# Performance work log

Hardware: AMD Instinct MI355X
Metric: run time of the kernel (lower is better)

The kernel has to match this reference:

```python
import jax, jax.numpy as jnp
import numpy as np

N_NODES = 100000
N_EDGES = 1600000
D_IN = 128
D_OUT = 128


def setup_inputs() -> dict:
    key = jax.random.key(0)
    k1, k2, k3 = jax.random.split(key, 3)
    x = jax.random.normal(k1, (N_NODES, D_IN), dtype=jnp.float32)
    edge_index = jax.random.randint(k2, (2, N_EDGES), 0, N_NODES, dtype=jnp.int64)
    # Xavier-uniform-like init for weight (matches nn.init.xavier_uniform_ scale)
    limit = float(np.sqrt(6.0 / (D_IN + D_OUT)))
    weight = jax.random.uniform(k3, (D_IN, D_OUT), dtype=jnp.float32,
                                minval=-limit, maxval=limit)
    bias = jnp.zeros((D_OUT,), dtype=jnp.float32)
    return {"x": x, "edge_index": edge_index, "weight": weight, "bias": bias}


def reference(x, edge_index, weight, bias):
    num_nodes = x.shape[0]
    src = edge_index[0]  # edge_index_i: gather side
    dst = edge_index[1]  # edge_index_j: scatter side

    # Degree of each node counted over src endpoints.
    deg = jax.ops.segment_sum(jnp.ones_like(src, dtype=x.dtype), src,
                              num_segments=num_nodes)
    # deg^{-1/2} with inf -> 0 for isolated nodes.
    deg_safe = jnp.where(deg > 0, deg, jnp.ones_like(deg))
    deg_inv_sqrt = jnp.where(deg > 0, jax.lax.rsqrt(deg_safe), jnp.zeros_like(deg))

    norm = deg_inv_sqrt[src] * deg_inv_sqrt[dst]  # [E]

    h = x @ weight  # [N, D_OUT]
    # Edge-parallel gather, scale, scatter-add.
    msgs = norm[:, None] * h[src]  # [E, D_OUT]
    out = jax.ops.segment_sum(msgs, dst, num_segments=num_nodes)  # [N, D_OUT]
    return out + bias
```

## Files before the change

kernel.cpp:

```cpp
#include <hip/hip_runtime.h>

#define D 128
#define CAP 64
#define STRIP_LOG 13
#define STRIP (1 << STRIP_LOG)
#define NCHUNK 32
#define LDK 132

typedef __attribute__((ext_vector_type(8))) short bf16x8;
typedef __attribute__((ext_vector_type(4))) float f32x4;

__device__ __forceinline__ unsigned f2bf(float f) {
    unsigned u = __float_as_uint(f);
    return (u + 0x7fffu + ((u >> 16) & 1u)) >> 16;
}

__device__ __forceinline__ int chunk_size(int n_edges) {
    return (((n_edges + NCHUNK - 1) / NCHUNK) + 3) & ~3;
}

__global__ __launch_bounds__(256) void k_histA(const int* __restrict__ src,
                                               const int* __restrict__ dst,
                                               int* __restrict__ pb_s,
                                               int* __restrict__ pb_d, int n_edges) {
    int strip = blockIdx.x / NCHUNK, chunk = blockIdx.x % NCHUNK;
    int lo = strip << STRIP_LOG;
    __shared__ int hs[STRIP];
    __shared__ int hd[STRIP];
    for (int i = threadIdx.x; i < STRIP; i += 256) { hs[i] = 0; hd[i] = 0; }
    __syncthreads();

    int csz = chunk_size(n_edges);
    int beg = chunk * csz;
    int end = min(beg + csz, n_edges);
    if (beg < end) {
        int aend = beg + ((end - beg) & ~3);
        for (int i = beg + threadIdx.x * 4; i + 3 < aend; i += 1024) {
            int4 s = *(const int4*)(src + i);
            int4 d = *(const int4*)(dst + i);
            unsigned b;
            b = (unsigned)(s.x - lo); if (b < STRIP) atomicAdd(&hs[b], 1);
            b = (unsigned)(s.y - lo); if (b < STRIP) atomicAdd(&hs[b], 1);
            b = (unsigned)(s.z - lo); if (b < STRIP) atomicAdd(&hs[b], 1);
            b = (unsigned)(s.w - lo); if (b < STRIP) atomicAdd(&hs[b], 1);
            b = (unsigned)(d.x - lo); if (b < STRIP) atomicAdd(&hd[b], 1);
            b = (unsigned)(d.y - lo); if (b < STRIP) atomicAdd(&hd[b], 1);
            b = (unsigned)(d.z - lo); if (b < STRIP) atomicAdd(&hd[b], 1);
            b = (unsigned)(d.w - lo); if (b < STRIP) atomicAdd(&hd[b], 1);
        }
        for (int e = aend + threadIdx.x; e < end; e += 256) {
            unsigned bs = (unsigned)(src[e] - lo); if (bs < STRIP) atomicAdd(&hs[bs], 1);
            unsigned bd = (unsigned)(dst[e] - lo); if (bd < STRIP) atomicAdd(&hd[bd], 1);
        }
    }
    __syncthreads();
    int* ps = pb_s + (size_t)blockIdx.x * STRIP;
    int* pd = pb_d + (size_t)blockIdx.x * STRIP;
    for (int i = threadIdx.x; i < STRIP; i += 256) { ps[i] = hs[i]; pd[i] = hd[i]; }
}

__global__ __launch_bounds__(256) void k_base_dis(int* __restrict__ pb_d,
                                                  const int* __restrict__ pb_s,
                                                  int* __restrict__ deg_dst,
                                                  float* __restrict__ dis,
                                                  int n, int nbins) {
    int g = blockIdx.x * 256 + threadIdx.x;
    if (g >= nbins) return;
    int strip = g >> STRIP_LOG, bin = g & (STRIP - 1);
    size_t base = (size_t)strip * NCHUNK * STRIP + bin;
    int run = 0;
    #pragma unroll
    for (int c = 0; c < NCHUNK; ++c) {
        size_t idx = base + (size_t)c * STRIP;
        int v = pb_d[idx];
        pb_d[idx] = run;
        run += v;
    }
    if (g < n) {
        deg_dst[g] = run;
        int ssum = 0;
        #pragma unroll
        for (int c = 0; c < NCHUNK; ++c) ssum += pb_s[base + (size_t)c * STRIP];
        dis[g] = (ssum > 0) ? rsqrtf((float)ssum) : 0.0f;
    }
}

__global__ __launch_bounds__(256) void k_placeB(const int* __restrict__ src,
                                                const int* __restrict__ dst,
                                                const int* __restrict__ pb_d,
                                                int* __restrict__ epad, int n_edges) {
    int strip = blockIdx.x / NCHUNK, chunk = blockIdx.x % NCHUNK;
    int lo = strip << STRIP_LOG;
    __shared__ int cur[STRIP];
    const int* cb = pb_d + (size_t)blockIdx.x * STRIP;
    for (int i = threadIdx.x; i < STRIP; i += 256) cur[i] = cb[i];
    __syncthreads();

    int csz = chunk_size(n_edges);
    int beg = chunk * csz;
    int end = min(beg + csz, n_edges);
    if (beg < end) {
        int aend = beg + ((end - beg) & ~3);
        for (int i = beg + threadIdx.x * 4; i + 3 < aend; i += 1024) {
            int4 s = *(const int4*)(src + i);
            int4 d = *(const int4*)(dst + i);
            unsigned b;
            b = (unsigned)(d.x - lo);
            if (b < STRIP) { int r = atomicAdd(&cur[b], 1); if (r < CAP) epad[(((unsigned)lo + b) << 6) + r] = s.x; }
            b = (unsigned)(d.y - lo);
            if (b < STRIP) { int r = atomicAdd(&cur[b], 1); if (r < CAP) epad[(((unsigned)lo + b) << 6) + r] = s.y; }
            b = (unsigned)(d.z - lo);
            if (b < STRIP) { int r = atomicAdd(&cur[b], 1); if (r < CAP) epad[(((unsigned)lo + b) << 6) + r] = s.z; }
            b = (unsigned)(d.w - lo);
            if (b < STRIP) { int r = atomicAdd(&cur[b], 1); if (r < CAP) epad[(((unsigned)lo + b) << 6) + r] = s.w; }
        }
        for (int e = aend + threadIdx.x; e < end; e += 256) {
            unsigned b = (unsigned)(dst[e] - lo);
            if (b < STRIP) { int r = atomicAdd(&cur[b], 1); if (r < CAP) epad[(((unsigned)lo + b) << 6) + r] = src[e]; }
        }
    }
}

__global__ __launch_bounds__(256) void k_gemm(const float* __restrict__ x,
                                              const float* __restrict__ w,
                                              const float* __restrict__ dis,
                                              unsigned* __restrict__ hb, int nrows) {
    __shared__ __align__(16) unsigned short smem[2][128][LDK];
    int tid = threadIdx.x;
    int row0 = blockIdx.x * 128;
    int nr = min(128, nrows - row0);

    {
        const float4* w4 = (const float4*)w;
        for (int i = tid; i < 128 * 32; i += 256) {
            int k = i >> 5, n0 = (i & 31) * 4;
            float4 v = w4[i];
            smem[1][n0 + 0][k] = (unsigned short)f2bf(v.x);
            smem[1][n0 + 1][k] = (unsigned short)f2bf(v.y);
            smem[1][n0 + 2][k] = (unsigned short)f2bf(v.z);
            smem[1][n0 + 3][k] = (unsigned short)f2bf(v.w);
        }
    }
    {
        const float4* x4 = (const float4*)(x + (size_t)row0 * D);
        for (int i = tid; i < 128 * 32; i += 256) {
            int r = i >> 5, c4 = (i & 31) * 4;
            float4 v = (r < nr) ? x4[i] : make_float4(0.f, 0.f, 0.f, 0.f);
            unsigned lo = f2bf(v.x) | (f2bf(v.y) << 16);
            unsigned hi = f2bf(v.z) | (f2bf(v.w) << 16);
            *(uint2*)&smem[0][r][c4] = make_uint2(lo, hi);
        }
    }
    __syncthreads();

    int lane = tid & 63, wv = tid >> 6;
    int m = lane & 15, quad = lane >> 4;
    int rbase = wv * 32;

    f32x4 acc[2][8] = {};
    #pragma unroll
    for (int kt = 0; kt < 4; ++kt) {
        int k0 = kt * 32 + quad * 8;
        bf16x8 a0 = *(const bf16x8*)&smem[0][rbase + m][k0];
        bf16x8 a1 = *(const bf16x8*)&smem[0][rbase + 16 + m][k0];
        bf16x8 b[8];
        #pragma unroll
        for (int ct = 0; ct < 8; ++ct)
            b[ct] = *(const bf16x8*)&smem[1][ct * 16 + m][k0];
        #pragma unroll
        for (int ct = 0; ct < 8; ++ct) {
            acc[0][ct] = __builtin_amdgcn_mfma_f32_16x16x32_bf16(a0, b[ct], acc[0][ct], 0, 0, 0);
            acc[1][ct] = __builtin_amdgcn_mfma_f32_16x16x32_bf16(a1, b[ct], acc[1][ct], 0, 0, 0);
        }
    }

    __syncthreads();
    float* sO = (float*)smem;
    #pragma unroll
    for (int rt = 0; rt < 2; ++rt)
        #pragma unroll
        for (int ct = 0; ct < 8; ++ct)
            #pragma unroll
            for (int reg = 0; reg < 4; ++reg)
                sO[(rbase + rt * 16 + quad * 4 + reg) * LDK + ct * 16 + m] = acc[rt][ct][reg];
    __syncthreads();

    int r = tid >> 1, hf = tid & 1;
    if (r < nr) {
        float dn = dis[row0 + r];
        const float* so = sO + r * LDK + hf * 64;
        unsigned* hrow = hb + (size_t)(row0 + r) * 64 + hf * 32;
        #pragma unroll
        for (int j = 0; j < 8; ++j) {
            float2 p0 = *(const float2*)(so + j * 8 + 0);
            float2 p1 = *(const float2*)(so + j * 8 + 2);
            float2 p2 = *(const float2*)(so + j * 8 + 4);
            float2 p3 = *(const float2*)(so + j * 8 + 6);
            uint4 o;
            o.x = f2bf(dn * p0.x) | (f2bf(dn * p0.y) << 16);
            o.y = f2bf(dn * p1.x) | (f2bf(dn * p1.y) << 16);
            o.z = f2bf(dn * p2.x) | (f2bf(dn * p2.y) << 16);
            o.w = f2bf(dn * p3.x) | (f2bf(dn * p3.y) << 16);
            *(uint4*)(hrow + j * 4) = o;
        }
    }
}

#define ACC8(u) do { \
    ax[0] += __uint_as_float((u).x << 16); ax[1] += __uint_as_float((u).x & 0xffff0000u); \
    ax[2] += __uint_as_float((u).y << 16); ax[3] += __uint_as_float((u).y & 0xffff0000u); \
    ax[4] += __uint_as_float((u).z << 16); ax[5] += __uint_as_float((u).z & 0xffff0000u); \
    ax[6] += __uint_as_float((u).w << 16); ax[7] += __uint_as_float((u).w & 0xffff0000u); } while (0)

__global__ __launch_bounds__(256) void k_accum(const int* __restrict__ epad,
                                               const int* __restrict__ degd,
                                               const uint4* __restrict__ hb4,
                                               const float* __restrict__ dis,
                                               const float* __restrict__ bias,
                                               float* __restrict__ out, int n) {
    int wid = threadIdx.x >> 6, lane = threadIdx.x & 63;
    int node = blockIdx.x * 4 + wid;
    if (node >= n) return;
    int deg = min(degd[node], CAP);
    int g = lane >> 4, c = lane & 15;
    const int* ep = epad + (size_t)node * CAP;

    float ax[8] = {0.f, 0.f, 0.f, 0.f, 0.f, 0.f, 0.f, 0.f};
    int e = g;
    for (; e + 12 < deg; e += 16) {
        int s0 = ep[e];
        int s1 = ep[e + 4];
        int s2 = ep[e + 8];
        int s3 = ep[e + 12];
        uint4 u0 = hb4[(size_t)s0 * 16 + c];
        uint4 u1 = hb4[(size_t)s1 * 16 + c];
        uint4 u2 = hb4[(size_t)s2 * 16 + c];
        uint4 u3 = hb4[(size_t)s3 * 16 + c];
        ACC8(u0); ACC8(u1); ACC8(u2); ACC8(u3);
    }
    for (; e < deg; e += 4) {
        int s0 = ep[e];
        uint4 u0 = hb4[(size_t)s0 * 16 + c];
        ACC8(u0);
    }

    #pragma unroll
    for (int k = 0; k < 8; ++k) {
        ax[k] += __shfl_xor(ax[k], 16, 64);
        ax[k] += __shfl_xor(ax[k], 32, 64);
    }

    if (g == 0) {
        float dn = dis[node];
        float4 b0 = ((const float4*)bias)[c * 2];
        float4 b1 = ((const float4*)bias)[c * 2 + 1];
        float4 o0 = make_float4(fmaf(dn, ax[0], b0.x), fmaf(dn, ax[1], b0.y),
                                fmaf(dn, ax[2], b0.z), fmaf(dn, ax[3], b0.w));
        float4 o1 = make_float4(fmaf(dn, ax[4], b1.x), fmaf(dn, ax[5], b1.y),
                                fmaf(dn, ax[6], b1.z), fmaf(dn, ax[7], b1.w));
        float4* op = (float4*)(out + (size_t)node * D) + c * 2;
        op[0] = o0;
        op[1] = o1;
    }
}

extern "C" void kernel_launch(void* const* d_in, const int* in_sizes, int n_in,
                              void* d_out, int out_size, void* d_ws, size_t ws_size,
                              hipStream_t stream) {
    const float* x    = (const float*)d_in[0];
    const int*   ei   = (const int*)d_in[1];
    const float* w    = (const float*)d_in[2];
    const float* bias = (const float*)d_in[3];
    float* out = (float*)d_out;

    int n_edges = in_sizes[1] / 2;
    int n_nodes = in_sizes[0] / D;
    const int* src = ei;
    const int* dst = ei + n_edges;

    int nstrips = (n_nodes + STRIP - 1) >> STRIP_LOG;
    int nbins = nstrips * STRIP;

    char* ws = (char*)d_ws;
    unsigned* hb = (unsigned*)ws;      ws += (size_t)n_nodes * 64 * sizeof(unsigned);
    int* epad    = (int*)ws;           ws += (size_t)n_nodes * CAP * sizeof(int);
    int* deg_dst = (int*)ws;           ws += (size_t)n_nodes * sizeof(int);
    float* dis   = (float*)ws;         ws += (size_t)n_nodes * sizeof(float);
    int* pb_s    = (int*)ws;           ws += (size_t)nstrips * NCHUNK * STRIP * sizeof(int);
    int* pb_d    = (int*)ws;

    k_histA<<<nstrips * NCHUNK, 256, 0, stream>>>(src, dst, pb_s, pb_d, n_edges);
    k_base_dis<<<(nbins + 255) / 256, 256, 0, stream>>>(pb_d, pb_s, deg_dst, dis,
                                                        n_nodes, nbins);
    k_gemm<<<(n_nodes + 127) / 128, 256, 0, stream>>>(x, w, dis, hb, n_nodes);
    k_placeB<<<nstrips * NCHUNK, 256, 0, stream>>>(src, dst, pb_d, epad, n_edges);
    k_accum<<<(n_nodes + 3) / 4, 256, 0, stream>>>(epad, deg_dst, (const uint4*)hb,
                                                   dis, bias, out, n_nodes);
}
```

Measured before the change: 283.0 us.

## Replace strip histogram and placement passes with single global-atomic placement kernel

Drops the strip-partitioned shared-memory histogram, prefix-base and placement kernels and replaces them with one edge-parallel kernel. It uses global atomics on per-node degree counters both to count source degrees and to assign slots in the padded destination adjacency. The rsqrt normalization is now computed on the fly from the integer degrees inside the GEMM and accumulate kernels. This removes two launches and the multiple re-reads of the edge lists. In exchange it relies on contended global atomics and leaves the in-slot edge order nondeterministic, so float summation order can vary between runs.

```diff
diff --git a/kernel.cpp b/kernel.cpp
--- a/kernel.cpp
+++ b/kernel.cpp
@@ -2,9 +2,6 @@
 
 #define D 128
 #define CAP 64
-#define STRIP_LOG 13
-#define STRIP (1 << STRIP_LOG)
-#define NCHUNK 32
 #define LDK 132
 
 typedef __attribute__((ext_vector_type(8))) short bf16x8;
@@ -15,115 +12,41 @@
     return (u + 0x7fffu + ((u >> 16) & 1u)) >> 16;
 }
 
-__device__ __forceinline__ int chunk_size(int n_edges) {
-    return (((n_edges + NCHUNK - 1) / NCHUNK) + 3) & ~3;
-}
-
-__global__ __launch_bounds__(256) void k_histA(const int* __restrict__ src,
+__device__ __forceinline__ float deg2dis(int dg) {
+    return (dg > 0) ? rsqrtf((float)dg) : 0.0f;
+}
+
+__global__ __launch_bounds__(256) void k_place(const int* __restrict__ src,
                                                const int* __restrict__ dst,
-                                               int* __restrict__ pb_s,
-                                               int* __restrict__ pb_d, int n_edges) {
-    int strip = blockIdx.x / NCHUNK, chunk = blockIdx.x % NCHUNK;
-    int lo = strip << STRIP_LOG;
-    __shared__ int hs[STRIP];
-    __shared__ int hd[STRIP];
-    for (int i = threadIdx.x; i < STRIP; i += 256) { hs[i] = 0; hd[i] = 0; }
-    __syncthreads();
-
-    int csz = chunk_size(n_edges);
-    int beg = chunk * csz;
-    int end = min(beg + csz, n_edges);
-    if (beg < end) {
-        int aend = beg + ((end - beg) & ~3);
-        for (int i = beg + threadIdx.x * 4; i + 3 < aend; i += 1024) {
-            int4 s = *(const int4*)(src + i);
-            int4 d = *(const int4*)(dst + i);
-            unsigned b;
-            b = (unsigned)(s.x - lo); if (b < STRIP) atomicAdd(&hs[b], 1);
-            b = (unsigned)(s.y - lo); if (b < STRIP) atomicAdd(&hs[b], 1);
-            b = (unsigned)(s.z - lo); if (b < STRIP) atomicAdd(&hs[b], 1);
-            b = (unsigned)(s.w - lo); if (b < STRIP) atomicAdd(&hs[b], 1);
-            b = (unsigned)(d.x - lo); if (b < STRIP) atomicAdd(&hd[b], 1);
-            b = (unsigned)(d.y - lo); if (b < STRIP) atomicAdd(&hd[b], 1);
-            b = (unsigned)(d.z - lo); if (b < STRIP) atomicAdd(&hd[b], 1);
-            b = (unsigned)(d.w - lo); if (b < STRIP) atomicAdd(&hd[b], 1);
-        }
-        for (int e = aend + threadIdx.x; e < end; e += 256) {
-            unsigned bs = (unsigned)(src[e] - lo); if (bs < STRIP) atomicAdd(&hs[bs], 1);
-            unsigned bd = (unsigned)(dst[e] - lo); if (bd < STRIP) atomicAdd(&hd[bd], 1);
-        }
-    }
-    __syncthreads();
-    int* ps = pb_s + (size_t)blockIdx.x * STRIP;
-    int* pd = pb_d + (size_t)blockIdx.x * STRIP;
-    for (int i = threadIdx.x; i < STRIP; i += 256) { ps[i] = hs[i]; pd[i] = hd[i]; }
-}
-
-__global__ __launch_bounds__(256) void k_base_dis(int* __restrict__ pb_d,
-                                                  const int* __restrict__ pb_s,
-                                                  int* __restrict__ deg_dst,
-                                                  float* __restrict__ dis,
-                                                  int n, int nbins) {
-    int g = blockIdx.x * 256 + threadIdx.x;
-    if (g >= nbins) return;
-    int strip = g >> STRIP_LOG, bin = g & (STRIP - 1);
-    size_t base = (size_t)strip * NCHUNK * STRIP + bin;
-    int run = 0;
-    #pragma unroll
-    for (int c = 0; c < NCHUNK; ++c) {
-        size_t idx = base + (size_t)c * STRIP;
-        int v = pb_d[idx];
-        pb_d[idx] = run;
-        run += v;
-    }
-    if (g < n) {
-        deg_dst[g] = run;
-        int ssum = 0;
-        #pragma unroll
-        for (int c = 0; c < NCHUNK; ++c) ssum += pb_s[base + (size_t)c * STRIP];
-        dis[g] = (ssum > 0) ? rsqrtf((float)ssum) : 0.0f;
-    }
-}
-
-__global__ __launch_bounds__(256) void k_placeB(const int* __restrict__ src,
-                                                const int* __restrict__ dst,
-                                                const int* __restrict__ pb_d,
-                                                int* __restrict__ epad, int n_edges) {
-    int strip = blockIdx.x / NCHUNK, chunk = blockIdx.x % NCHUNK;
-    int lo = strip << STRIP_LOG;
-    __shared__ int cur[STRIP];
-    const int* cb = pb_d + (size_t)blockIdx.x * STRIP;
-    for (int i = threadIdx.x; i < STRIP; i += 256) cur[i] = cb[i];
-    __syncthreads();
-
-    int csz = chunk_size(n_edges);
-    int beg = chunk * csz;
-    int end = min(beg + csz, n_edges);
-    if (beg < end) {
-        int aend = beg + ((end - beg) & ~3);
-        for (int i = beg + threadIdx.x * 4; i + 3 < aend; i += 1024) {
-            int4 s = *(const int4*)(src + i);
-            int4 d = *(const int4*)(dst + i);
-            unsigned b;
-            b = (unsigned)(d.x - lo);
-            if (b < STRIP) { int r = atomicAdd(&cur[b], 1); if (r < CAP) epad[(((unsigned)lo + b) << 6) + r] = s.x; }
-            b = (unsigned)(d.y - lo);
-            if (b < STRIP) { int r = atomicAdd(&cur[b], 1); if (r < CAP) epad[(((unsigned)lo + b) << 6) + r] = s.y; }
-            b = (unsigned)(d.z - lo);
-            if (b < STRIP) { int r = atomicAdd(&cur[b], 1); if (r < CAP) epad[(((unsigned)lo + b) << 6) + r] = s.z; }
-            b = (unsigned)(d.w - lo);
-            if (b < STRIP) { int r = atomicAdd(&cur[b], 1); if (r < CAP) epad[(((unsigned)lo + b) << 6) + r] = s.w; }
-        }
-        for (int e = aend + threadIdx.x; e < end; e += 256) {
-            unsigned b = (unsigned)(dst[e] - lo);
-            if (b < STRIP) { int r = atomicAdd(&cur[b], 1); if (r < CAP) epad[(((unsigned)lo + b) << 6) + r] = src[e]; }
+                                               int* __restrict__ deg_s,
+                                               int* __restrict__ deg_d,
+                                               int* __restrict__ epad, int n_edges) {
+    int i = (blockIdx.x * 256 + threadIdx.x) * 4;
+    if (i + 3 < n_edges) {
+        int4 s = *(const int4*)(src + i);
+        int4 d = *(const int4*)(dst + i);
+        atomicAdd(&deg_s[s.x], 1);
+        atomicAdd(&deg_s[s.y], 1);
+        atomicAdd(&deg_s[s.z], 1);
+        atomicAdd(&deg_s[s.w], 1);
+        int r;
+        r = atomicAdd(&deg_d[d.x], 1); if (r < CAP) epad[((size_t)d.x << 6) + r] = s.x;
+        r = atomicAdd(&deg_d[d.y], 1); if (r < CAP) epad[((size_t)d.y << 6) + r] = s.y;
+        r = atomicAdd(&deg_d[d.z], 1); if (r < CAP) epad[((size_t)d.z << 6) + r] = s.z;
+        r = atomicAdd(&deg_d[d.w], 1); if (r < CAP) epad[((size_t)d.w << 6) + r] = s.w;
+    } else {
+        for (; i < n_edges; ++i) {
+            int sv = src[i], dv = dst[i];
+            atomicAdd(&deg_s[sv], 1);
+            int r = atomicAdd(&deg_d[dv], 1);
+            if (r < CAP) epad[((size_t)dv << 6) + r] = sv;
         }
     }
 }
 
 __global__ __launch_bounds__(256) void k_gemm(const float* __restrict__ x,
                                               const float* __restrict__ w,
-                                              const float* __restrict__ dis,
+                                              const int* __restrict__ degs,
                                               unsigned* __restrict__ hb, int nrows) {
     __shared__ __align__(16) unsigned short smem[2][128][LDK];
     int tid = threadIdx.x;
@@ -187,7 +110,7 @@
 
     int r = tid >> 1, hf = tid & 1;
     if (r < nr) {
-        float dn = dis[row0 + r];
+        float dn = deg2dis(degs[row0 + r]);
         const float* so = sO + r * LDK + hf * 64;
         unsigned* hrow = hb + (size_t)(row0 + r) * 64 + hf * 32;
         #pragma unroll
@@ -215,7 +138,7 @@
 __global__ __launch_bounds__(256) void k_accum(const int* __restrict__ epad,
                                                const int* __restrict__ degd,
                                                const uint4* __restrict__ hb4,
-                                               const float* __restrict__ dis,
+                                               const int* __restrict__ degs,
                                                const float* __restrict__ bias,
                                                float* __restrict__ out, int n) {
     int wid = threadIdx.x >> 6, lane = threadIdx.x & 63;
@@ -251,7 +174,7 @@
     }
 
     if (g == 0) {
-        float dn = dis[node];
+        float dn = deg2dis(degs[node]);
         float4 b0 = ((const float4*)bias)[c * 2];
         float4 b1 = ((const float4*)bias)[c * 2 + 1];
         float4 o0 = make_float4(fmaf(dn, ax[0], b0.x), fmaf(dn, ax[1], b0.y),
@@ -278,22 +201,16 @@
     const int* src = ei;
     const int* dst = ei + n_edges;
 
-    int nstrips = (n_nodes + STRIP - 1) >> STRIP_LOG;
-    int nbins = nstrips * STRIP;
-
     char* ws = (char*)d_ws;
-    unsigned* hb = (unsigned*)ws;      ws += (size_t)n_nodes * 64 * sizeof(unsigned);
-    int* epad    = (int*)ws;           ws += (size_t)n_nodes * CAP * sizeof(int);
-    int* deg_dst = (int*)ws;           ws += (size_t)n_nodes * sizeof(int);
-    float* dis   = (float*)ws;         ws += (size_t)n_nodes * sizeof(float);
-    int* pb_s    = (int*)ws;           ws += (size_t)nstrips * NCHUNK * STRIP * sizeof(int);
-    int* pb_d    = (int*)ws;
-
-    k_histA<<<nstrips * NCHUNK, 256, 0, stream>>>(src, dst, pb_s, pb_d, n_edges);
-    k_base_dis<<<(nbins + 255) / 256, 256, 0, stream>>>(pb_d, pb_s, deg_dst, dis,
-                                                        n_nodes, nbins);
-    k_gemm<<<(n_nodes + 127) / 128, 256, 0, stream>>>(x, w, dis, hb, n_nodes);
-    k_placeB<<<nstrips * NCHUNK, 256, 0, stream>>>(src, dst, pb_d, epad, n_edges);
-    k_accum<<<(n_nodes + 3) / 4, 256, 0, stream>>>(epad, deg_dst, (const uint4*)hb,
-                                                   dis, bias, out, n_nodes);
-}
+    unsigned* hb = (unsigned*)ws;  ws += (size_t)n_nodes * 64 * sizeof(unsigned);
+    int* epad    = (int*)ws;       ws += (size_t)n_nodes * CAP * sizeof(int);
+    int* deg_s   = (int*)ws;       ws += (size_t)n_nodes * sizeof(int);
+    int* deg_d   = (int*)ws;
+
+    hipMemsetAsync(deg_s, 0, (size_t)2 * n_nodes * sizeof(int), stream);
+    k_place<<<(n_edges + 1023) / 1024, 256, 0, stream>>>(src, dst, deg_s, deg_d,
+                                                         epad, n_edges);
+    k_gemm<<<(n_nodes + 127) / 128, 256, 0, stream>>>(x, w, deg_s, hb, n_nodes);
+    k_accum<<<(n_nodes + 3) / 4, 256, 0, stream>>>(epad, deg_d, (const uint4*)hb,
+                                                   deg_s, bias, out, n_nodes);
+}
```

Measured after the change: 355.7 us. 25.7% more time.

## Pack four 8-bit bin counters per LDS word to widen strips

Applied to the files above, without the earlier changes.

Histogram and placement counters now hold four 8-bit bins per 32-bit word, using shifted atomic adds in shared memory. The same LDS budget therefore covers four times as many nodes per strip. This cuts the number of strips, and so the number of full passes over the edge list in the histogram and placement kernels. NCHUNK rises to keep enough blocks. The risk is that any per-node running count above 255 would overflow into the neighbouring byte, which holds only while node degrees stay small.

```diff
diff --git a/kernel.cpp b/kernel.cpp
--- a/kernel.cpp
+++ b/kernel.cpp
@@ -2,9 +2,11 @@
 
 #define D 128
 #define CAP 64
-#define STRIP_LOG 13
+#define STRIP_LOG 15
 #define STRIP (1 << STRIP_LOG)
-#define NCHUNK 32
+#define WORDS_LOG (STRIP_LOG - 2)
+#define WORDS (1 << WORDS_LOG)
+#define NCHUNK 128
 #define LDK 132
 
 typedef __attribute__((ext_vector_type(8))) short bf16x8;
@@ -21,13 +23,13 @@
 
 __global__ __launch_bounds__(256) void k_histA(const int* __restrict__ src,
                                                const int* __restrict__ dst,
-                                               int* __restrict__ pb_s,
-                                               int* __restrict__ pb_d, int n_edges) {
+                                               unsigned* __restrict__ pb_s,
+                                               unsigned* __restrict__ pb_d, int n_edges) {
     int strip = blockIdx.x / NCHUNK, chunk = blockIdx.x % NCHUNK;
     int lo = strip << STRIP_LOG;
-    __shared__ int hs[STRIP];
-    __shared__ int hd[STRIP];
-    for (int i = threadIdx.x; i < STRIP; i += 256) { hs[i] = 0; hd[i] = 0; }
+    __shared__ unsigned hs[WORDS];
+    __shared__ unsigned hd[WORDS];
+    for (int i = threadIdx.x; i < WORDS; i += 256) { hs[i] = 0; hd[i] = 0; }
     __syncthreads();
 
     int csz = chunk_size(n_edges);
@@ -39,61 +41,83 @@
             int4 s = *(const int4*)(src + i);
             int4 d = *(const int4*)(dst + i);
             unsigned b;
-            b = (unsigned)(s.x - lo); if (b < STRIP) atomicAdd(&hs[b], 1);
-            b = (unsigned)(s.y - lo); if (b < STRIP) atomicAdd(&hs[b], 1);
-            b = (unsigned)(s.z - lo); if (b < STRIP) atomicAdd(&hs[b], 1);
-            b = (unsigned)(s.w - lo); if (b < STRIP) atomicAdd(&hs[b], 1);
-            b = (unsigned)(d.x - lo); if (b < STRIP) atomicAdd(&hd[b], 1);
-            b = (unsigned)(d.y - lo); if (b < STRIP) atomicAdd(&hd[b], 1);
-            b = (unsigned)(d.z - lo); if (b < STRIP) atomicAdd(&hd[b], 1);
-            b = (unsigned)(d.w - lo); if (b < STRIP) atomicAdd(&hd[b], 1);
+            b = (unsigned)(s.x - lo); if (b < STRIP) atomicAdd(&hs[b >> 2], 1u << ((b & 3) * 8));
+            b = (unsigned)(s.y - lo); if (b < STRIP) atomicAdd(&hs[b >> 2], 1u << ((b & 3) * 8));
+            b = (unsigned)(s.z - lo); if (b < STRIP) atomicAdd(&hs[b >> 2], 1u << ((b & 3) * 8));
+            b = (unsigned)(s.w - lo); if (b < STRIP) atomicAdd(&hs[b >> 2], 1u << ((b & 3) * 8));
+            b = (unsigned)(d.x - lo); if (b < STRIP) atomicAdd(&hd[b >> 2], 1u << ((b & 3) * 8));
+            b = (unsigned)(d.y - lo); if (b < STRIP) atomicAdd(&hd[b >> 2], 1u << ((b & 3) * 8));
+            b = (unsigned)(d.z - lo); if (b < STRIP) atomicAdd(&hd[b >> 2], 1u << ((b & 3) * 8));
+            b = (unsigned)(d.w - lo); if (b < STRIP) atomicAdd(&hd[b >> 2], 1u << ((b & 3) * 8));
         }
         for (int e = aend + threadIdx.x; e < end; e += 256) {
-            unsigned bs = (unsigned)(src[e] - lo); if (bs < STRIP) atomicAdd(&hs[bs], 1);
-            unsigned bd = (unsigned)(dst[e] - lo); if (bd < STRIP) atomicAdd(&hd[bd], 1);
-        }
-    }
-    __syncthreads();
-    int* ps = pb_s + (size_t)blockIdx.x * STRIP;
-    int* pd = pb_d + (size_t)blockIdx.x * STRIP;
-    for (int i = threadIdx.x; i < STRIP; i += 256) { ps[i] = hs[i]; pd[i] = hd[i]; }
-}
-
-__global__ __launch_bounds__(256) void k_base_dis(int* __restrict__ pb_d,
-                                                  const int* __restrict__ pb_s,
+            unsigned bs = (unsigned)(src[e] - lo);
+            if (bs < STRIP) atomicAdd(&hs[bs >> 2], 1u << ((bs & 3) * 8));
+            unsigned bd = (unsigned)(dst[e] - lo);
+            if (bd < STRIP) atomicAdd(&hd[bd >> 2], 1u << ((bd & 3) * 8));
+        }
+    }
+    __syncthreads();
+    unsigned* ps = pb_s + (size_t)blockIdx.x * WORDS;
+    unsigned* pd = pb_d + (size_t)blockIdx.x * WORDS;
+    for (int i = threadIdx.x; i < WORDS; i += 256) { ps[i] = hs[i]; pd[i] = hd[i]; }
+}
+
+__global__ __launch_bounds__(256) void k_base_dis(unsigned* __restrict__ pb_d,
+                                                  const unsigned* __restrict__ pb_s,
                                                   int* __restrict__ deg_dst,
                                                   float* __restrict__ dis,
-                                                  int n, int nbins) {
-    int g = blockIdx.x * 256 + threadIdx.x;
-    if (g >= nbins) return;
-    int strip = g >> STRIP_LOG, bin = g & (STRIP - 1);
-    size_t base = (size_t)strip * NCHUNK * STRIP + bin;
-    int run = 0;
-    #pragma unroll
+                                                  int n, int nwords) {
+    int gw = blockIdx.x * 256 + threadIdx.x;
+    if (gw >= nwords) return;
+    int strip = gw >> WORDS_LOG, widx = gw & (WORDS - 1);
+    size_t base = (size_t)strip * NCHUNK * WORDS + widx;
+
+    unsigned run[4] = {0, 0, 0, 0};
     for (int c = 0; c < NCHUNK; ++c) {
-        size_t idx = base + (size_t)c * STRIP;
-        int v = pb_d[idx];
-        pb_d[idx] = run;
-        run += v;
-    }
-    if (g < n) {
-        deg_dst[g] = run;
-        int ssum = 0;
-        #pragma unroll
-        for (int c = 0; c < NCHUNK; ++c) ssum += pb_s[base + (size_t)c * STRIP];
-        dis[g] = (ssum > 0) ? rsqrtf((float)ssum) : 0.0f;
+        size_t idx = base + (size_t)c * WORDS;
+        unsigned v = pb_d[idx];
+        pb_d[idx] = run[0] | (run[1] << 8) | (run[2] << 16) | (run[3] << 24);
+        run[0] += v & 0xffu;
+        run[1] += (v >> 8) & 0xffu;
+        run[2] += (v >> 16) & 0xffu;
+        run[3] += (v >> 24) & 0xffu;
+    }
+    int g0 = (strip << STRIP_LOG) + widx * 4;
+    if (g0 >= n) return;
+
+    unsigned ss[4] = {0, 0, 0, 0};
+    for (int c = 0; c < NCHUNK; ++c) {
+        unsigned v = pb_s[base + (size_t)c * WORDS];
+        ss[0] += v & 0xffu;
+        ss[1] += (v >> 8) & 0xffu;
+        ss[2] += (v >> 16) & 0xffu;
+        ss[3] += (v >> 24) & 0xffu;
+    }
+    if (g0 + 3 < n) {
+        *(int4*)(deg_dst + g0) = make_int4(run[0], run[1], run[2], run[3]);
+        *(float4*)(dis + g0) = make_float4(
+            ss[0] ? rsqrtf((float)ss[0]) : 0.0f, ss[1] ? rsqrtf((float)ss[1]) : 0.0f,
+            ss[2] ? rsqrtf((float)ss[2]) : 0.0f, ss[3] ? rsqrtf((float)ss[3]) : 0.0f);
+    } else {
+        #pragma unroll
+        for (int j = 0; j < 4; ++j)
+            if (g0 + j < n) {
+                deg_dst[g0 + j] = run[j];
+                dis[g0 + j] = ss[j] ? rsqrtf((float)ss[j]) : 0.0f;
+            }
     }
 }
 
 __global__ __launch_bounds__(256) void k_placeB(const int* __restrict__ src,
                                                 const int* __restrict__ dst,
-                                                const int* __restrict__ pb_d,
+                                                const unsigned* __restrict__ pb_d,
                                                 int* __restrict__ epad, int n_edges) {
     int strip = blockIdx.x / NCHUNK, chunk = blockIdx.x % NCHUNK;
     int lo = strip << STRIP_LOG;
-    __shared__ int cur[STRIP];
-    const int* cb = pb_d + (size_t)blockIdx.x * STRIP;
-    for (int i = threadIdx.x; i < STRIP; i += 256) cur[i] = cb[i];
+    __shared__ unsigned cur[WORDS];
+    const unsigned* cb = pb_d + (size_t)blockIdx.x * WORDS;
+    for (int i = threadIdx.x; i < WORDS; i += 256) cur[i] = cb[i];
     __syncthreads();
 
     int csz = chunk_size(n_edges);
@@ -104,19 +128,39 @@
         for (int i = beg + threadIdx.x * 4; i + 3 < aend; i += 1024) {
             int4 s = *(const int4*)(src + i);
             int4 d = *(const int4*)(dst + i);
-            unsigned b;
+            unsigned b, o, r;
             b = (unsigned)(d.x - lo);
-            if (b < STRIP) { int r = atomicAdd(&cur[b], 1); if (r < CAP) epad[(((unsigned)lo + b) << 6) + r] = s.x; }
+            if (b < STRIP) {
+                o = atomicAdd(&cur[b >> 2], 1u << ((b & 3) * 8));
+                r = (o >> ((b & 3) * 8)) & 0xffu;
+                if (r < CAP) epad[(((unsigned)lo + b) << 6) + r] = s.x;
+            }
             b = (unsigned)(d.y - lo);
-            if (b < STRIP) { int r = atomicAdd(&cur[b], 1); if (r < CAP) epad[(((unsigned)lo + b) << 6) + r] = s.y; }
+            if (b < STRIP) {
+                o = atomicAdd(&cur[b >> 2], 1u << ((b & 3) * 8));
+                r = (o >> ((b & 3) * 8)) & 0xffu;
+                if (r < CAP) epad[(((unsigned)lo + b) << 6) + r] = s.y;
+            }
             b = (unsigned)(d.z - lo);
-            if (b < STRIP) { int r = atomicAdd(&cur[b], 1); if (r < CAP) epad[(((unsigned)lo + b) << 6) + r] = s.z; }
+            if (b < STRIP) {
+                o = atomicAdd(&cur[b >> 2], 1u << ((b & 3) * 8));
+                r = (o >> ((b & 3) * 8)) & 0xffu;
+                if (r < CAP) epad[(((unsigned)lo + b) << 6) + r] = s.z;
+            }
             b = (unsigned)(d.w - lo);
-            if (b < STRIP) { int r = atomicAdd(&cur[b], 1); if (r < CAP) epad[(((unsigned)lo + b) << 6) + r] = s.w; }
+            if (b < STRIP) {
+                o = atomicAdd(&cur[b >> 2], 1u << ((b & 3) * 8));
+                r = (o >> ((b & 3) * 8)) & 0xffu;
+                if (r < CAP) epad[(((unsigned)lo + b) << 6) + r] = s.w;
+            }
         }
         for (int e = aend + threadIdx.x; e < end; e += 256) {
             unsigned b = (unsigned)(dst[e] - lo);
-            if (b < STRIP) { int r = atomicAdd(&cur[b], 1); if (r < CAP) epad[(((unsigned)lo + b) << 6) + r] = src[e]; }
+            if (b < STRIP) {
+                unsigned o = atomicAdd(&cur[b >> 2], 1u << ((b & 3) * 8));
+                unsigned r = (o >> ((b & 3) * 8)) & 0xffu;
+                if (r < CAP) epad[(((unsigned)lo + b) << 6) + r] = src[e];
+            }
         }
     }
 }
@@ -279,19 +323,19 @@
     const int* dst = ei + n_edges;
 
     int nstrips = (n_nodes + STRIP - 1) >> STRIP_LOG;
-    int nbins = nstrips * STRIP;
+    int nwords = nstrips * WORDS;
 
     char* ws = (char*)d_ws;
     unsigned* hb = (unsigned*)ws;      ws += (size_t)n_nodes * 64 * sizeof(unsigned);
     int* epad    = (int*)ws;           ws += (size_t)n_nodes * CAP * sizeof(int);
     int* deg_dst = (int*)ws;           ws += (size_t)n_nodes * sizeof(int);
     float* dis   = (float*)ws;         ws += (size_t)n_nodes * sizeof(float);
-    int* pb_s    = (int*)ws;           ws += (size_t)nstrips * NCHUNK * STRIP * sizeof(int);
-    int* pb_d    = (int*)ws;
+    unsigned* pb_s = (unsigned*)ws;    ws += (size_t)nstrips * NCHUNK * WORDS * sizeof(unsigned);
+    unsigned* pb_d = (unsigned*)ws;
 
     k_histA<<<nstrips * NCHUNK, 256, 0, stream>>>(src, dst, pb_s, pb_d, n_edges);
-    k_base_dis<<<(nbins + 255) / 256, 256, 0, stream>>>(pb_d, pb_s, deg_dst, dis,
-                                                        n_nodes, nbins);
+    k_base_dis<<<(nwords + 255) / 256, 256, 0, stream>>>(pb_d, pb_s, deg_dst, dis,
+                                                         n_nodes, nwords);
     k_gemm<<<(n_nodes + 127) / 128, 256, 0, stream>>>(x, w, dis, hb, n_nodes);
     k_placeB<<<nstrips * NCHUNK, 256, 0, stream>>>(src, dst, pb_d, epad, n_edges);
     k_accum<<<(n_nodes + 3) / 4, 256, 0, stream>>>(epad, deg_dst, (const uint4*)hb,
```

After: 261.1 us. -7.7%, faster.
